# Kernel tuning notes

Hardware: AMD Instinct MI355X
Metric: run time of the kernel (lower is better)

Reference implementation:

```python
import jax, jax.numpy as jnp
import numpy as np

B, H, W, C = 4, 128, 128, 64
MODES, SCHMIDT = 16, 4


def setup_inputs() -> dict:
    key = jax.random.key(0)
    k1, k2, k3 = jax.random.split(key, 3)
    # glorot-like scale for (M, M, C, C, S) weights: fan over modes*modes*C
    w_scale = float(np.sqrt(2.0 / (MODES * MODES * C + MODES * MODES * C)))
    return {
        "x": jax.random.normal(k1, (B, H, W, C), dtype=jnp.float32),
        "weights_real": jax.random.normal(k2, (MODES, MODES, C, C, SCHMIDT), dtype=jnp.float32) * w_scale,
        "weights_imag": jax.random.normal(k3, (MODES, MODES, C, C, SCHMIDT), dtype=jnp.float32) * w_scale,
        "modes": MODES,
        "schmidt_rank": SCHMIDT,
    }


def reference(x, weights_real, weights_imag, modes, schmidt_rank):
    # x: [B, H, W, C] real
    b, h, w, c = x.shape
    # quantum_fourier_modes: spatial Fourier transform truncated to `modes` per dim
    x_ft = jnp.fft.fftn(x, axes=(1, 2))[:, :modes, :modes, :]  # [B, M, M, C] complex64
    weights = weights_real + 1j * weights_imag                 # [M, M, C, O, S]
    # 'b...nc,mncos->b...mos' with ellipsis = first mode axis (k)
    out_ft = jnp.einsum("bknc,mncos->bkmos", x_ft, weights)    # [B, M, M, O, S]
    # Schmidt-rank recombination: sum over schmidt axis (normalized)
    out_modes = out_ft.sum(axis=-1) / float(np.sqrt(schmidt_rank))  # [B, M, M, O]
    o = out_modes.shape[-1]
    # inverse quantum_fourier_modes: zero-pad low modes back to full grid, inverse FFT
    full = jnp.zeros((b, h, w, o), dtype=out_modes.dtype)
    full = full.at[:, :modes, :modes, :].set(out_modes)
    out = jnp.fft.ifftn(full, axes=(1, 2))
    return out.real
```

## Files before the change

### kernel.cpp

```cpp
#include <hip/hip_runtime.h>


static constexpr int BATCH = 4;

static constexpr size_t TMP_OFF = 0;
static constexpr size_t XFT_OFF = 1048576;
static constexpr size_t OMT_OFF = 1179648;

__device__ __forceinline__ void init_trig_lds(float2* twl) {
    if (threadIdx.x < 128) {
        float s, c;
        sincosf(6.283185307179586f * (float)threadIdx.x * 0.0078125f, &s, &c);
        twl[threadIdx.x] = make_float2(c, s);
    }
}

__global__ __launch_bounds__(256) void k_dft_w(const float* __restrict__ x,
                                               float2* __restrict__ tmp1) {
    __shared__ float4 xs[2048];
    __shared__ float2 twl[128];
    init_trig_lds(twl);
    const int bid = blockIdx.x;
    const float4* x4 = reinterpret_cast<const float4*>(x) + (size_t)bid * 2048;
    #pragma unroll
    for (int i = 0; i < 8; ++i) xs[threadIdx.x + 256 * i] = x4[threadIdx.x + 256 * i];
    __syncthreads();
    const int n  = threadIdx.x >> 4;
    const int c4 = threadIdx.x & 15;
    float4 ar = make_float4(0.f, 0.f, 0.f, 0.f);
    float4 ai = make_float4(0.f, 0.f, 0.f, 0.f);
    int t = 0;
    #pragma unroll 8
    for (int w = 0; w < 128; ++w) {
        const float4 v  = xs[w * 16 + c4];
        const float2 tw = twl[t];
        t = (t + n) & 127;
        ar.x += v.x * tw.x; ai.x -= v.x * tw.y;
        ar.y += v.y * tw.x; ai.y -= v.y * tw.y;
        ar.z += v.z * tw.x; ai.z -= v.z * tw.y;
        ar.w += v.w * tw.x; ai.w -= v.w * tw.y;
    }
    float4* o = reinterpret_cast<float4*>(tmp1 + ((size_t)bid * 16 + n) * 64 + c4 * 4);
    o[0] = make_float4(ar.x, ai.x, ar.y, ai.y);
    o[1] = make_float4(ar.z, ai.z, ar.w, ai.w);
}

__global__ __launch_bounds__(256) void k_dft_h(const float2* __restrict__ tmp1,
                                               float2* __restrict__ xft) {
    __shared__ float2 twl[128];
    init_trig_lds(twl);
    __syncthreads();
    const int tid = blockIdx.x * 256 + threadIdx.x;
    const int c = tid & 63;
    const int n = (tid >> 6) & 15;
    const int k = (tid >> 10) & 15;
    const int b = tid >> 14;
    const float2* src = tmp1 + (size_t)b * 131072 + n * 64 + c;
    float2 acc = make_float2(0.f, 0.f);
    int t = 0;
    #pragma unroll 8
    for (int h = 0; h < 128; ++h) {
        const float2 a  = src[(size_t)h * 1024];
        const float2 tw = twl[t];
        t = (t + k) & 127;
        acc.x += a.x * tw.x + a.y * tw.y;
        acc.y += a.y * tw.x - a.x * tw.y;
    }
    xft[(size_t)(b * 16 + k) * 1024 + n * 64 + c] = acc;
}

__global__ __launch_bounds__(256) void k_gemm2(const float2* __restrict__ xft,
                                               const float* __restrict__ wr,
                                               const float* __restrict__ wi,
                                               float2* __restrict__ omT) {
    __shared__ float2 Bs[4096];
    const int oq = blockIdx.x & 15;
    const int m  = blockIdx.x >> 4;
    #pragma unroll
    for (int i = 0; i < 16; ++i) {
        const int idx = threadIdx.x + 256 * i;
        const int nn = idx >> 8, cc = (idx >> 2) & 63, oo = idx & 3;
        const size_t wb = ((size_t)((m * 16 + nn) * 64 + cc) * 64 + oq * 4 + oo) * 4;
        const float4 r4 = *reinterpret_cast<const float4*>(wr + wb);
        const float4 i4 = *reinterpret_cast<const float4*>(wi + wb);
        Bs[idx] = make_float2((r4.x + r4.y + r4.z + r4.w) * 0.5f,
                              (i4.x + i4.y + i4.z + i4.w) * 0.5f);
    }
    __syncthreads();
    const int ol = threadIdx.x & 3;
    const int r  = threadIdx.x >> 2;
    const float4* xr = reinterpret_cast<const float4*>(xft + (size_t)r * 1024);
    float accx = 0.f, accy = 0.f;
    #pragma unroll 8
    for (int k2 = 0; k2 < 512; ++k2) {
        const float4 a  = xr[k2];
        const float2 b0 = Bs[8 * k2 + ol];
        const float2 b1 = Bs[8 * k2 + 4 + ol];
        accx += a.x * b0.x - a.y * b0.y + a.z * b1.x - a.w * b1.y;
        accy += a.x * b0.y + a.y * b0.x + a.z * b1.y + a.w * b1.x;
    }
    const int b = r >> 4, k = r & 15;
    const int o = oq * 4 + ol;
    omT[(((size_t)b * 16 + m) * 64 + o) * 16 + k] = make_float2(accx, accy);
}

__global__ __launch_bounds__(256) void k_idft(const float2* __restrict__ omT,
                                              float* __restrict__ out) {
    __shared__ float2 u_s[1024];
    __shared__ float2 twl[128];
    init_trig_lds(twl);
    const int bid = blockIdx.x;
    const int h = bid & 127, b = bid >> 7;
    __syncthreads();
    #pragma unroll
    for (int i = 0; i < 4; ++i) {
        const int e = threadIdx.x + 256 * i;
        const float4* src = reinterpret_cast<const float4*>(
            omT + (((size_t)b * 16 + (e >> 6)) * 64 + (e & 63)) * 16);
        float re = 0.f, im = 0.f;
        int t = 0;
        #pragma unroll
        for (int k8 = 0; k8 < 8; ++k8) {
            const float4 q = src[k8];
            const float2 tw0 = twl[t]; t = (t + h) & 127;
            const float2 tw1 = twl[t]; t = (t + h) & 127;
            re += q.x * tw0.x - q.y * tw0.y + q.z * tw1.x - q.w * tw1.y;
            im += q.x * tw0.y + q.y * tw0.x + q.z * tw1.y + q.w * tw1.x;
        }
        u_s[e] = make_float2(re, im);
    }
    __syncthreads();
    const int o4 = threadIdx.x & 15;
    const int wg = threadIdx.x >> 4;
    const float inv = 1.0f / 16384.0f;
    #pragma unroll
    for (int i = 0; i < 8; ++i) {
        const int w = wg * 8 + i;
        float4 acc = make_float4(0.f, 0.f, 0.f, 0.f);
        int t = 0;
        #pragma unroll
        for (int mm = 0; mm < 16; ++mm) {
            const float2 tw  = twl[t];
            t = (t + w) & 127;
            const float4 u01 = *reinterpret_cast<const float4*>(&u_s[mm * 64 + o4 * 4]);
            const float4 u23 = *reinterpret_cast<const float4*>(&u_s[mm * 64 + o4 * 4 + 2]);
            acc.x += u01.x * tw.x - u01.y * tw.y;
            acc.y += u01.z * tw.x - u01.w * tw.y;
            acc.z += u23.x * tw.x - u23.y * tw.y;
            acc.w += u23.z * tw.x - u23.w * tw.y;
        }
        acc.x *= inv; acc.y *= inv; acc.z *= inv; acc.w *= inv;
        *reinterpret_cast<float4*>(out + ((size_t)bid * 128 + w) * 64 + o4 * 4) = acc;
    }
}

extern "C" void kernel_launch(void* const* d_in, const int* in_sizes, int n_in,
                              void* d_out, int out_size, void* d_ws, size_t ws_size,
                              hipStream_t stream) {
    const float* x  = (const float*)d_in[0];
    const float* wr = (const float*)d_in[1];
    const float* wi = (const float*)d_in[2];
    float* out = (float*)d_out;
    float* ws  = (float*)d_ws;

    float2* tmp1 = (float2*)(ws + TMP_OFF);
    float2* xft  = (float2*)(ws + XFT_OFF);
    float2* omT  = (float2*)(ws + OMT_OFF);

    k_dft_w<<<BATCH * 128, 256, 0, stream>>>(x, tmp1);
    k_dft_h<<<256, 256, 0, stream>>>(tmp1, xft);
    k_gemm2<<<256, 256, 0, stream>>>(xft, wr, wi, omT);
    k_idft <<<BATCH * 128, 256, 0, stream>>>(omT, out);
}
```

Baseline: 168.3 us.

## Replace twiddle LDS tables with recurrence rotations and split reductions across threads

Twiddle factors now come from a per-thread complex rotation recurrence instead of a shared-memory sincos table, which removes the table setup and one barrier in each DFT kernel. The H-direction DFT splits the 128-point sum across two half-blocks, doubling the grid and combining the halves through LDS. The GEMM kernel uses 512 threads per block and splits K in two, merging the halves with a shuffle. The inverse DFT caches u values in registers. The recurrences can accumulate float rounding error, and the extra register use may lower occupancy.

New measurement: 161.0 us. 1.04x faster.

```diff
diff --git a/kernel.cpp b/kernel.cpp
--- a/kernel.cpp
+++ b/kernel.cpp
@@ -2,43 +2,41 @@
 
 
 static constexpr int BATCH = 4;
+static constexpr float STEP_C = 0.9987954562051724f;
+static constexpr float STEP_S = 0.04906767432741801f;
 
 static constexpr size_t TMP_OFF = 0;
 static constexpr size_t XFT_OFF = 1048576;
 static constexpr size_t OMT_OFF = 1179648;
 
-__device__ __forceinline__ void init_trig_lds(float2* twl) {
-    if (threadIdx.x < 128) {
-        float s, c;
-        sincosf(6.283185307179586f * (float)threadIdx.x * 0.0078125f, &s, &c);
-        twl[threadIdx.x] = make_float2(c, s);
-    }
+__device__ __forceinline__ float2 cmulp(float2 a, float2 b) {
+    return make_float2(a.x * b.x - a.y * b.y, a.x * b.y + a.y * b.x);
 }
 
 __global__ __launch_bounds__(256) void k_dft_w(const float* __restrict__ x,
                                                float2* __restrict__ tmp1) {
     __shared__ float4 xs[2048];
-    __shared__ float2 twl[128];
-    init_trig_lds(twl);
     const int bid = blockIdx.x;
     const float4* x4 = reinterpret_cast<const float4*>(x) + (size_t)bid * 2048;
     #pragma unroll
     for (int i = 0; i < 8; ++i) xs[threadIdx.x + 256 * i] = x4[threadIdx.x + 256 * i];
-    __syncthreads();
     const int n  = threadIdx.x >> 4;
     const int c4 = threadIdx.x & 15;
+    float rs, rc;
+    sincosf(6.283185307179586f * (float)n * 0.0078125f, &rs, &rc);
+    const float2 rot = make_float2(rc, rs);
+    __syncthreads();
     float4 ar = make_float4(0.f, 0.f, 0.f, 0.f);
     float4 ai = make_float4(0.f, 0.f, 0.f, 0.f);
-    int t = 0;
+    float2 tw = make_float2(1.f, 0.f);
     #pragma unroll 8
     for (int w = 0; w < 128; ++w) {
-        const float4 v  = xs[w * 16 + c4];
-        const float2 tw = twl[t];
-        t = (t + n) & 127;
+        const float4 v = xs[w * 16 + c4];
         ar.x += v.x * tw.x; ai.x -= v.x * tw.y;
         ar.y += v.y * tw.x; ai.y -= v.y * tw.y;
         ar.z += v.z * tw.x; ai.z -= v.z * tw.y;
         ar.w += v.w * tw.x; ai.w -= v.w * tw.y;
+        tw = cmulp(tw, rot);
     }
     float4* o = reinterpret_cast<float4*>(tmp1 + ((size_t)bid * 16 + n) * 64 + c4 * 4);
     o[0] = make_float4(ar.x, ai.x, ar.y, ai.y);
@@ -47,29 +45,38 @@
 
 __global__ __launch_bounds__(256) void k_dft_h(const float2* __restrict__ tmp1,
                                                float2* __restrict__ xft) {
-    __shared__ float2 twl[128];
-    init_trig_lds(twl);
-    __syncthreads();
-    const int tid = blockIdx.x * 256 + threadIdx.x;
-    const int c = tid & 63;
-    const int n = (tid >> 6) & 15;
-    const int k = (tid >> 10) & 15;
-    const int b = tid >> 14;
-    const float2* src = tmp1 + (size_t)b * 131072 + n * 64 + c;
+    __shared__ float2 red[128];
+    const int bid = blockIdx.x;
+    const int nh = bid & 7;
+    const int k  = (bid >> 3) & 15;
+    const int b  = bid >> 7;
+    const int ol = threadIdx.x & 127;
+    const int hs = threadIdx.x >> 7;
+    const int c  = ol & 63;
+    const int n  = nh * 2 + (ol >> 6);
+    float rs, rc;
+    sincosf(6.283185307179586f * (float)k * 0.0078125f, &rs, &rc);
+    const float2 rot = make_float2(rc, rs);
+    float2 tw = make_float2((hs && (k & 1)) ? -1.f : 1.f, 0.f);
+    const float2* src = tmp1 + (size_t)b * 131072 + n * 64 + c + (size_t)hs * 65536;
     float2 acc = make_float2(0.f, 0.f);
-    int t = 0;
     #pragma unroll 8
-    for (int h = 0; h < 128; ++h) {
-        const float2 a  = src[(size_t)h * 1024];
-        const float2 tw = twl[t];
-        t = (t + k) & 127;
+    for (int j = 0; j < 64; ++j) {
+        const float2 a = src[(size_t)j * 1024];
         acc.x += a.x * tw.x + a.y * tw.y;
         acc.y += a.y * tw.x - a.x * tw.y;
+        tw = cmulp(tw, rot);
     }
-    xft[(size_t)(b * 16 + k) * 1024 + n * 64 + c] = acc;
+    if (hs) red[ol] = acc;
+    __syncthreads();
+    if (!hs) {
+        const float2 r = red[ol];
+        acc.x += r.x; acc.y += r.y;
+        xft[(size_t)(b * 16 + k) * 1024 + n * 64 + c] = acc;
+    }
 }
 
-__global__ __launch_bounds__(256) void k_gemm2(const float2* __restrict__ xft,
+__global__ __launch_bounds__(512) void k_gemm2(const float2* __restrict__ xft,
                                                const float* __restrict__ wr,
                                                const float* __restrict__ wi,
                                                float2* __restrict__ omT) {
@@ -77,8 +84,8 @@
     const int oq = blockIdx.x & 15;
     const int m  = blockIdx.x >> 4;
     #pragma unroll
-    for (int i = 0; i < 16; ++i) {
-        const int idx = threadIdx.x + 256 * i;
+    for (int i = 0; i < 8; ++i) {
+        const int idx = threadIdx.x + 512 * i;
         const int nn = idx >> 8, cc = (idx >> 2) & 63, oo = idx & 3;
         const size_t wb = ((size_t)((m * 16 + nn) * 64 + cc) * 64 + oq * 4 + oo) * 4;
         const float4 r4 = *reinterpret_cast<const float4*>(wr + wb);
@@ -87,70 +94,85 @@
                               (i4.x + i4.y + i4.z + i4.w) * 0.5f);
     }
     __syncthreads();
-    const int ol = threadIdx.x & 3;
-    const int r  = threadIdx.x >> 2;
-    const float4* xr = reinterpret_cast<const float4*>(xft + (size_t)r * 1024);
+    const int r  = threadIdx.x >> 3;
+    const int ol = (threadIdx.x >> 1) & 3;
+    const int ks = threadIdx.x & 1;
+    const float4* xr = reinterpret_cast<const float4*>(xft + (size_t)r * 1024) + ks * 256;
     float accx = 0.f, accy = 0.f;
     #pragma unroll 8
-    for (int k2 = 0; k2 < 512; ++k2) {
+    for (int k2 = 0; k2 < 256; ++k2) {
         const float4 a  = xr[k2];
-        const float2 b0 = Bs[8 * k2 + ol];
-        const float2 b1 = Bs[8 * k2 + 4 + ol];
+        const int base = 8 * (ks * 256 + k2);
+        const float2 b0 = Bs[base + ol];
+        const float2 b1 = Bs[base + 4 + ol];
         accx += a.x * b0.x - a.y * b0.y + a.z * b1.x - a.w * b1.y;
         accy += a.x * b0.y + a.y * b0.x + a.z * b1.y + a.w * b1.x;
     }
-    const int b = r >> 4, k = r & 15;
-    const int o = oq * 4 + ol;
-    omT[(((size_t)b * 16 + m) * 64 + o) * 16 + k] = make_float2(accx, accy);
+    accx += __shfl_xor(accx, 1);
+    accy += __shfl_xor(accy, 1);
+    if (ks == 0) {
+        const int b = r >> 4, k = r & 15;
+        const int o = oq * 4 + ol;
+        omT[(((size_t)b * 16 + m) * 64 + o) * 16 + k] = make_float2(accx, accy);
+    }
 }
 
 __global__ __launch_bounds__(256) void k_idft(const float2* __restrict__ omT,
                                               float* __restrict__ out) {
     __shared__ float2 u_s[1024];
-    __shared__ float2 twl[128];
-    init_trig_lds(twl);
     const int bid = blockIdx.x;
     const int h = bid & 127, b = bid >> 7;
-    __syncthreads();
+    float hs_, hc_;
+    sincosf(6.283185307179586f * (float)h * 0.0078125f, &hs_, &hc_);
+    const float2 rotk = make_float2(hc_, hs_);
     #pragma unroll
     for (int i = 0; i < 4; ++i) {
         const int e = threadIdx.x + 256 * i;
         const float4* src = reinterpret_cast<const float4*>(
             omT + (((size_t)b * 16 + (e >> 6)) * 64 + (e & 63)) * 16);
         float re = 0.f, im = 0.f;
-        int t = 0;
+        float2 tw = make_float2(1.f, 0.f);
         #pragma unroll
         for (int k8 = 0; k8 < 8; ++k8) {
             const float4 q = src[k8];
-            const float2 tw0 = twl[t]; t = (t + h) & 127;
-            const float2 tw1 = twl[t]; t = (t + h) & 127;
-            re += q.x * tw0.x - q.y * tw0.y + q.z * tw1.x - q.w * tw1.y;
-            im += q.x * tw0.y + q.y * tw0.x + q.z * tw1.y + q.w * tw1.x;
+            re += q.x * tw.x - q.y * tw.y; im += q.x * tw.y + q.y * tw.x;
+            tw = cmulp(tw, rotk);
+            re += q.z * tw.x - q.w * tw.y; im += q.z * tw.y + q.w * tw.x;
+            tw = cmulp(tw, rotk);
         }
         u_s[e] = make_float2(re, im);
     }
     __syncthreads();
     const int o4 = threadIdx.x & 15;
     const int wg = threadIdx.x >> 4;
+    float4 va[16], vb[16];
+    #pragma unroll
+    for (int mm = 0; mm < 16; ++mm) {
+        const float4* up = reinterpret_cast<const float4*>(&u_s[mm * 64 + o4 * 4]);
+        va[mm] = up[0];
+        vb[mm] = up[1];
+    }
+    float ws_, wc_;
+    sincosf(6.283185307179586f * (float)(wg * 8) * 0.0078125f, &ws_, &wc_);
+    float2 rotm = make_float2(wc_, ws_);
+    const float2 step = make_float2(STEP_C, STEP_S);
     const float inv = 1.0f / 16384.0f;
     #pragma unroll
     for (int i = 0; i < 8; ++i) {
         const int w = wg * 8 + i;
         float4 acc = make_float4(0.f, 0.f, 0.f, 0.f);
-        int t = 0;
+        float2 tw = make_float2(1.f, 0.f);
         #pragma unroll
         for (int mm = 0; mm < 16; ++mm) {
-            const float2 tw  = twl[t];
-            t = (t + w) & 127;
-            const float4 u01 = *reinterpret_cast<const float4*>(&u_s[mm * 64 + o4 * 4]);
-            const float4 u23 = *reinterpret_cast<const float4*>(&u_s[mm * 64 + o4 * 4 + 2]);
-            acc.x += u01.x * tw.x - u01.y * tw.y;
-            acc.y += u01.z * tw.x - u01.w * tw.y;
-            acc.z += u23.x * tw.x - u23.y * tw.y;
-            acc.w += u23.z * tw.x - u23.w * tw.y;
+            acc.x += va[mm].x * tw.x - va[mm].y * tw.y;
+            acc.y += va[mm].z * tw.x - va[mm].w * tw.y;
+            acc.z += vb[mm].x * tw.x - vb[mm].y * tw.y;
+            acc.w += vb[mm].z * tw.x - vb[mm].w * tw.y;
+            tw = cmulp(tw, rotm);
         }
         acc.x *= inv; acc.y *= inv; acc.z *= inv; acc.w *= inv;
         *reinterpret_cast<float4*>(out + ((size_t)bid * 128 + w) * 64 + o4 * 4) = acc;
+        rotm = cmulp(rotm, step);
     }
 }
 
@@ -168,7 +190,7 @@
     float2* omT  = (float2*)(ws + OMT_OFF);
 
     k_dft_w<<<BATCH * 128, 256, 0, stream>>>(x, tmp1);
-    k_dft_h<<<256, 256, 0, stream>>>(tmp1, xft);
-    k_gemm2<<<256, 256, 0, stream>>>(xft, wr, wi, omT);
+    k_dft_h<<<512, 256, 0, stream>>>(tmp1, xft);
+    k_gemm2<<<256, 512, 0, stream>>>(xft, wr, wi, omT);
     k_idft <<<BATCH * 128, 256, 0, stream>>>(omT, out);
 }
```
